# Kernel optimization log

Measured on AMD Instinct MI355X. Metric: run time of the kernel, lower is better.

The kernel has to match this reference:

```python
import jax, jax.numpy as jnp
import numpy as np

N = 100000
E = 600000
D = 128
D_OUT = 128
NUM_CONV = 3


def setup_inputs() -> dict:
    key = jax.random.key(0)
    k0, k1, k2, k3, k4, k5 = jax.random.split(key, 6)
    x = jax.random.normal(k0, (N, D), dtype=jnp.float32)
    edge_index = jax.random.randint(k1, (2, E), 0, N, dtype=jnp.int64)
    s = 1.0 / np.sqrt(D)
    W = jax.random.uniform(k2, (D, D), minval=-s, maxval=s, dtype=jnp.float32)
    b = jax.random.uniform(k3, (D,), minval=-s, maxval=s, dtype=jnp.float32)
    W_out = jax.random.uniform(k4, (D, D_OUT), minval=-s, maxval=s, dtype=jnp.float32)
    b_out = jax.random.uniform(k5, (D_OUT,), minval=-s, maxval=s, dtype=jnp.float32)
    return {"x": x, "edge_index": edge_index, "W": W, "b": b,
            "W_out": W_out, "b_out": b_out}


def reference(x, edge_index, W, b, W_out, b_out):
    src, dst = edge_index[0], edge_index[1]
    for _ in range(NUM_CONV):
        # gather messages from src nodes, scatter-sum into dst nodes
        agg = jax.ops.segment_sum(x[src], dst, num_segments=N)  # [N, D]
        x = jax.nn.relu(agg @ W + b)  # shared GCNLayer weights + ReLU
    return x @ W_out + b_out  # [N, D_OUT]
```

## Files before the change

### kernel.cpp

```cpp
#include <hip/hip_runtime.h>

#define NN 100000
#define NE 600000
#define DD 128


__global__ __launch_bounds__(256) void zero_kernel(int* __restrict__ p, int n) {
  int i = blockIdx.x * 256 + threadIdx.x;
  if (i < n) p[i] = 0;
}

__global__ __launch_bounds__(256) void count_deg(const int* __restrict__ dst, int* __restrict__ cnt) {
  int e = blockIdx.x * 256 + threadIdx.x;
  if (e < NE) atomicAdd(&cnt[dst[e]], 1);
}

__global__ __launch_bounds__(1024) void scan_partial(const int* __restrict__ cnt,
                                                     int* __restrict__ rowptr,
                                                     int* __restrict__ bsum) {
  __shared__ int tmp[2][1024];
  int t = threadIdx.x;
  int g = blockIdx.x * 1024 + t;
  int v = (g < NN) ? cnt[g] : 0;
  tmp[0][t] = v;
  __syncthreads();
  int pb = 0;
  for (int off = 1; off < 1024; off <<= 1) {
    int nv = tmp[pb][t] + ((t >= off) ? tmp[pb][t - off] : 0);
    tmp[1 - pb][t] = nv;
    pb ^= 1;
    __syncthreads();
  }
  int incl = tmp[pb][t];
  if (g < NN) rowptr[g] = incl - v;
  if (t == 1023) bsum[blockIdx.x] = incl;
}

__global__ void scan_sums(int* __restrict__ bsum, int nb) {
  if (threadIdx.x == 0 && blockIdx.x == 0) {
    int run = 0;
    for (int j = 0; j < nb; ++j) { int tv = bsum[j]; bsum[j] = run; run += tv; }
  }
}

__global__ __launch_bounds__(256) void scan_add(int* __restrict__ rowptr, const int* __restrict__ bsum) {
  int g = blockIdx.x * 256 + threadIdx.x;
  if (g < NN) rowptr[g] += bsum[g >> 10];
  if (g == 0) rowptr[NN] = NE;
}

__global__ __launch_bounds__(256) void fill_csr(const int* __restrict__ src, const int* __restrict__ dst,
                                                const int* __restrict__ rowptr, int* __restrict__ cur,
                                                int* __restrict__ srcidx) {
  int e = blockIdx.x * 256 + threadIdx.x;
  if (e < NE) {
    int d = dst[e];
    int pos = atomicAdd(&cur[d], 1);
    srcidx[rowptr[d] + pos] = src[e];
  }
}


__global__ __launch_bounds__(256) void aggregate(const float* __restrict__ y,
                                                 const int* __restrict__ rowptr,
                                                 const int* __restrict__ srcidx,
                                                 float* __restrict__ agg) {
  int grp  = (int)((blockIdx.x * 256 + threadIdx.x) >> 5);
  int lane = threadIdx.x & 31;
  if (grp >= NN) return;
  int beg = rowptr[grp], end = rowptr[grp + 1];
  float4 a0 = make_float4(0.f, 0.f, 0.f, 0.f);
  float4 a1 = make_float4(0.f, 0.f, 0.f, 0.f);
  int j = beg;
  for (; j + 2 <= end; j += 2) {
    int s0 = srcidx[j], s1 = srcidx[j + 1];
    float4 v0 = *(const float4*)(y + (size_t)s0 * DD + lane * 4);
    float4 v1 = *(const float4*)(y + (size_t)s1 * DD + lane * 4);
    a0.x += v0.x; a0.y += v0.y; a0.z += v0.z; a0.w += v0.w;
    a1.x += v1.x; a1.y += v1.y; a1.z += v1.z; a1.w += v1.w;
  }
  if (j < end) {
    int s0 = srcidx[j];
    float4 v0 = *(const float4*)(y + (size_t)s0 * DD + lane * 4);
    a0.x += v0.x; a0.y += v0.y; a0.z += v0.z; a0.w += v0.w;
  }
  float4 o = make_float4(a0.x + a1.x, a0.y + a1.y, a0.z + a1.z, a0.w + a1.w);
  *(float4*)(agg + (size_t)grp * DD + lane * 4) = o;
}


template <bool RELU>
__global__ __launch_bounds__(256) void gemm128(const float* __restrict__ A,
                                               const float* __restrict__ Wm,
                                               const float* __restrict__ bias,
                                               float* __restrict__ C, int nrows) {
  __shared__ float AsT[32][68];
  __shared__ float Ws[32][128];
  int t  = threadIdx.x;
  int tx = t & 15;
  int ty = t >> 4;
  int m0 = blockIdx.x * 64;
  float acc[4][8];
  #pragma unroll
  for (int r = 0; r < 4; ++r)
    #pragma unroll
    for (int c = 0; c < 8; ++c) acc[r][c] = 0.f;

  for (int kb = 0; kb < 4; ++kb) {
    #pragma unroll
    for (int i = 0; i < 2; ++i) {
      int q = t + i * 256;
      int m = q >> 3, k4 = q & 7;
      int row = m0 + m; if (row >= nrows) row = nrows - 1;
      float4 v = *(const float4*)(A + (size_t)row * DD + kb * 32 + k4 * 4);
      AsT[k4 * 4 + 0][m] = v.x;
      AsT[k4 * 4 + 1][m] = v.y;
      AsT[k4 * 4 + 2][m] = v.z;
      AsT[k4 * 4 + 3][m] = v.w;
    }
    #pragma unroll
    for (int i = 0; i < 4; ++i) {
      int q = t + i * 256;
      int kk = q >> 5, c4 = q & 31;
      *(float4*)(&Ws[kk][c4 * 4]) = *(const float4*)(Wm + (size_t)(kb * 32 + kk) * DD + c4 * 4);
    }
    __syncthreads();
    #pragma unroll
    for (int k = 0; k < 32; ++k) {
      float4 av = *(const float4*)(&AsT[k][ty * 4]);
      float4 w0 = *(const float4*)(&Ws[k][tx * 8]);
      float4 w1 = *(const float4*)(&Ws[k][tx * 8 + 4]);
      float a[4] = {av.x, av.y, av.z, av.w};
      float w[8] = {w0.x, w0.y, w0.z, w0.w, w1.x, w1.y, w1.z, w1.w};
      #pragma unroll
      for (int r = 0; r < 4; ++r)
        #pragma unroll
        for (int c = 0; c < 8; ++c) acc[r][c] += a[r] * w[c];
    }
    __syncthreads();
  }

  int c0 = tx * 8;
  float4 b0 = *(const float4*)(bias + c0);
  float4 b1 = *(const float4*)(bias + c0 + 4);
  float bb[8] = {b0.x, b0.y, b0.z, b0.w, b1.x, b1.y, b1.z, b1.w};
  #pragma unroll
  for (int r = 0; r < 4; ++r) {
    int row = m0 + ty * 4 + r;
    if (row < nrows) {
      float o[8];
      #pragma unroll
      for (int c = 0; c < 8; ++c) {
        float v = acc[r][c] + bb[c];
        o[c] = RELU ? fmaxf(v, 0.f) : v;
      }
      *(float4*)(C + (size_t)row * DD + c0)     = make_float4(o[0], o[1], o[2], o[3]);
      *(float4*)(C + (size_t)row * DD + c0 + 4) = make_float4(o[4], o[5], o[6], o[7]);
    }
  }
}


extern "C" void kernel_launch(void* const* d_in, const int* in_sizes, int n_in,
                              void* d_out, int out_size, void* d_ws, size_t ws_size,
                              hipStream_t stream) {
  const float* x     = (const float*)d_in[0];
  const int*   ei    = (const int*)d_in[1];
  const float* W     = (const float*)d_in[2];
  const float* b     = (const float*)d_in[3];
  const float* W_out = (const float*)d_in[4];
  const float* b_out = (const float*)d_in[5];
  float*       out   = (float*)d_out;

  const int* src = ei;
  const int* dst = ei + NE;

  char* ws = (char*)d_ws;
  int*   rowptr = (int*)(ws + 0);
  int*   cnt    = (int*)(ws + 400128);
  int*   bsum   = (int*)(ws + 800256);
  int*   srcidx = (int*)(ws + 802304);
  float* bufA   = (float*)(ws + 3202304);
  float* bufB   = (float*)(ws + 54402304);

  const int nb_scan = (NN + 1023) / 1024;

  zero_kernel<<<(NN + 255) / 256, 256, 0, stream>>>(cnt, NN);
  count_deg<<<(NE + 255) / 256, 256, 0, stream>>>(dst, cnt);
  scan_partial<<<nb_scan, 1024, 0, stream>>>(cnt, rowptr, bsum);
  scan_sums<<<1, 64, 0, stream>>>(bsum, nb_scan);
  scan_add<<<(NN + 255) / 256, 256, 0, stream>>>(rowptr, bsum);
  zero_kernel<<<(NN + 255) / 256, 256, 0, stream>>>(cnt, NN);
  fill_csr<<<(NE + 255) / 256, 256, 0, stream>>>(src, dst, rowptr, cnt, srcidx);

  const int aggBlocks  = (NN * 32 + 255) / 256;
  const int gemmBlocks = (NN + 63) / 64;

  aggregate<<<aggBlocks, 256, 0, stream>>>(x, rowptr, srcidx, bufA);
  gemm128<true><<<gemmBlocks, 256, 0, stream>>>(bufA, W, b, bufB, NN);
  aggregate<<<aggBlocks, 256, 0, stream>>>(bufB, rowptr, srcidx, bufA);
  gemm128<true><<<gemmBlocks, 256, 0, stream>>>(bufA, W, b, bufB, NN);
  aggregate<<<aggBlocks, 256, 0, stream>>>(bufB, rowptr, srcidx, bufA);
  gemm128<true><<<gemmBlocks, 256, 0, stream>>>(bufA, W, b, bufB, NN);
  gemm128<false><<<gemmBlocks, 256, 0, stream>>>(bufB, W_out, b_out, out, NN);
}
```

Measured before the change: 512.6 us.

## Replace FP32 SIMT GEMM with split-bf16 MFMA GEMM and bf16 hi/lo activations

Replaces the scalar FP32 GEMM with a matrix-core kernel that uses bf16x3 splitting (hi*hi + hi*lo + lo*hi) to keep near-FP32 accuracy. Aggregation now writes hi/lo bf16 halves directly, and the weights are pre-transposed and split once per call. The third layer writes its output in place as bf16 hi/lo, which feeds the output projection directly. Also moves the block-sum scan into shared memory. This triples the MFMA work and adds hi/lo traffic in exchange for much higher matrix-core throughput. The third layer's in-place overwrite of its input buffer relies on each block reading only its own rows.

```diff
diff --git a/kernel.cpp b/kernel.cpp
--- a/kernel.cpp
+++ b/kernel.cpp
@@ -3,6 +3,15 @@
 #define NN 100000
 #define NE 600000
 #define DD 128
+
+typedef __attribute__((ext_vector_type(8))) short bf16x8;
+typedef __attribute__((ext_vector_type(4))) float f32x4;
+
+__device__ __forceinline__ ushort f2bf(float f) {
+  uint u = __float_as_uint(f);
+  return (ushort)((u + 0x7FFF + ((u >> 16) & 1)) >> 16);
+}
+__device__ __forceinline__ float bf2f(ushort h) { return __uint_as_float(((uint)h) << 16); }
 
 
 __global__ __launch_bounds__(256) void zero_kernel(int* __restrict__ p, int n) {
@@ -36,11 +45,17 @@
   if (t == 1023) bsum[blockIdx.x] = incl;
 }
 
-__global__ void scan_sums(int* __restrict__ bsum, int nb) {
-  if (threadIdx.x == 0 && blockIdx.x == 0) {
+__global__ __launch_bounds__(128) void scan_sums(int* __restrict__ bsum, int nb) {
+  __shared__ int s[128];
+  int t = threadIdx.x;
+  s[t] = (t < nb) ? bsum[t] : 0;
+  __syncthreads();
+  if (t == 0) {
     int run = 0;
-    for (int j = 0; j < nb; ++j) { int tv = bsum[j]; bsum[j] = run; run += tv; }
-  }
+    for (int j = 0; j < nb; ++j) { int v = s[j]; s[j] = run; run += v; }
+  }
+  __syncthreads();
+  if (t < nb) bsum[t] = s[t];
 }
 
 __global__ __launch_bounds__(256) void scan_add(int* __restrict__ rowptr, const int* __restrict__ bsum) {
@@ -61,10 +76,25 @@
 }
 
 
+__global__ __launch_bounds__(256) void wprep(const float* __restrict__ W, const float* __restrict__ Wo,
+                                             ushort* __restrict__ WTh, ushort* __restrict__ WTl,
+                                             ushort* __restrict__ WToh, ushort* __restrict__ WTol) {
+  int i = blockIdx.x * 256 + threadIdx.x;
+  int j = i & 16383;
+  int k = j >> 7, n = j & 127;
+  float w = (i < 16384) ? W[j] : Wo[j];
+  ushort h = f2bf(w);
+  ushort lo = f2bf(w - bf2f(h));
+  int o = n * 128 + k;
+  if (i < 16384) { WTh[o] = h; WTl[o] = lo; }
+  else           { WToh[o] = h; WTol[o] = lo; }
+}
+
+
 __global__ __launch_bounds__(256) void aggregate(const float* __restrict__ y,
                                                  const int* __restrict__ rowptr,
                                                  const int* __restrict__ srcidx,
-                                                 float* __restrict__ agg) {
+                                                 ushort* __restrict__ Ah, ushort* __restrict__ Al) {
   int grp  = (int)((blockIdx.x * 256 + threadIdx.x) >> 5);
   int lane = threadIdx.x & 31;
   if (grp >= NN) return;
@@ -84,78 +114,100 @@
     float4 v0 = *(const float4*)(y + (size_t)s0 * DD + lane * 4);
     a0.x += v0.x; a0.y += v0.y; a0.z += v0.z; a0.w += v0.w;
   }
-  float4 o = make_float4(a0.x + a1.x, a0.y + a1.y, a0.z + a1.z, a0.w + a1.w);
-  *(float4*)(agg + (size_t)grp * DD + lane * 4) = o;
-}
-
-
-template <bool RELU>
-__global__ __launch_bounds__(256) void gemm128(const float* __restrict__ A,
-                                               const float* __restrict__ Wm,
-                                               const float* __restrict__ bias,
-                                               float* __restrict__ C, int nrows) {
-  __shared__ float AsT[32][68];
-  __shared__ float Ws[32][128];
-  int t  = threadIdx.x;
-  int tx = t & 15;
-  int ty = t >> 4;
-  int m0 = blockIdx.x * 64;
-  float acc[4][8];
-  #pragma unroll
-  for (int r = 0; r < 4; ++r)
-    #pragma unroll
-    for (int c = 0; c < 8; ++c) acc[r][c] = 0.f;
-
-  for (int kb = 0; kb < 4; ++kb) {
-    #pragma unroll
-    for (int i = 0; i < 2; ++i) {
-      int q = t + i * 256;
-      int m = q >> 3, k4 = q & 7;
-      int row = m0 + m; if (row >= nrows) row = nrows - 1;
-      float4 v = *(const float4*)(A + (size_t)row * DD + kb * 32 + k4 * 4);
-      AsT[k4 * 4 + 0][m] = v.x;
-      AsT[k4 * 4 + 1][m] = v.y;
-      AsT[k4 * 4 + 2][m] = v.z;
-      AsT[k4 * 4 + 3][m] = v.w;
-    }
+  float v[4] = {a0.x + a1.x, a0.y + a1.y, a0.z + a1.z, a0.w + a1.w};
+  ushort h[4], l[4];
+  #pragma unroll
+  for (int r = 0; r < 4; ++r) { h[r] = f2bf(v[r]); l[r] = f2bf(v[r] - bf2f(h[r])); }
+  uint2 hh, ll;
+  hh.x = (uint)h[0] | ((uint)h[1] << 16); hh.y = (uint)h[2] | ((uint)h[3] << 16);
+  ll.x = (uint)l[0] | ((uint)l[1] << 16); ll.y = (uint)l[2] | ((uint)l[3] << 16);
+  *(uint2*)(Ah + (size_t)grp * DD + lane * 4) = hh;
+  *(uint2*)(Al + (size_t)grp * DD + lane * 4) = ll;
+}
+
+
+template <int MODE>
+__global__ __launch_bounds__(256, 3) void gemm_mfma(const ushort* Ah, const ushort* Al,
+                                                    const ushort* __restrict__ Bh, const ushort* __restrict__ Bl,
+                                                    const float* __restrict__ bias,
+                                                    float* Cf, ushort* Ch, ushort* Cl, int nrows) {
+  __shared__ ushort BHs[128 * 64];
+  __shared__ ushort BLs[128 * 64];
+  int t = threadIdx.x;
+  int w = t >> 6, l = t & 63;
+  int lrow = l & 15, g = l >> 4;
+  int m0 = blockIdx.x * 128 + w * 32;
+
+  f32x4 acc[2][8];
+  #pragma unroll
+  for (int rt = 0; rt < 2; ++rt)
+    #pragma unroll
+    for (int ct = 0; ct < 8; ++ct) acc[rt][ct] = (f32x4){0.f, 0.f, 0.f, 0.f};
+
+  #pragma unroll
+  for (int p = 0; p < 2; ++p) {
     #pragma unroll
     for (int i = 0; i < 4; ++i) {
-      int q = t + i * 256;
-      int kk = q >> 5, c4 = q & 31;
-      *(float4*)(&Ws[kk][c4 * 4]) = *(const float4*)(Wm + (size_t)(kb * 32 + kk) * DD + c4 * 4);
+      int c = t + i * 256;
+      int n = c >> 3, k8 = c & 7;
+      int gsrc = n * 128 + p * 64 + k8 * 8;
+      int dsw  = n * 64 + (((k8 * 16) ^ ((n & 7) << 4)) >> 1);
+      *(uint4*)(&BHs[dsw]) = *(const uint4*)(Bh + gsrc);
+      *(uint4*)(&BLs[dsw]) = *(const uint4*)(Bl + gsrc);
     }
     __syncthreads();
-    #pragma unroll
-    for (int k = 0; k < 32; ++k) {
-      float4 av = *(const float4*)(&AsT[k][ty * 4]);
-      float4 w0 = *(const float4*)(&Ws[k][tx * 8]);
-      float4 w1 = *(const float4*)(&Ws[k][tx * 8 + 4]);
-      float a[4] = {av.x, av.y, av.z, av.w};
-      float w[8] = {w0.x, w0.y, w0.z, w0.w, w1.x, w1.y, w1.z, w1.w};
+
+    #pragma unroll
+    for (int kb = 0; kb < 2; ++kb) {
+      int kgl = (p * 2 + kb) * 32 + g * 8;
+      bf16x8 ah[2], al[2];
       #pragma unroll
-      for (int r = 0; r < 4; ++r)
+      for (int rt = 0; rt < 2; ++rt) {
+        int row = m0 + rt * 16 + lrow; if (row >= nrows) row = nrows - 1;
+        ah[rt] = *(const bf16x8*)(Ah + (size_t)row * DD + kgl);
+        al[rt] = *(const bf16x8*)(Al + (size_t)row * DD + kgl);
+      }
+      int kloc = kb * 64 + g * 16;
+      int swz = (lrow & 7) << 4;
+      #pragma unroll
+      for (int ct = 0; ct < 8; ++ct) {
+        int off = (ct * 16 + lrow) * 64 + ((kloc ^ swz) >> 1);
+        bf16x8 bh = *(const bf16x8*)(&BHs[off]);
+        bf16x8 bl = *(const bf16x8*)(&BLs[off]);
         #pragma unroll
-        for (int c = 0; c < 8; ++c) acc[r][c] += a[r] * w[c];
+        for (int rt = 0; rt < 2; ++rt) {
+          acc[rt][ct] = __builtin_amdgcn_mfma_f32_16x16x32_bf16(ah[rt], bh, acc[rt][ct], 0, 0, 0);
+          acc[rt][ct] = __builtin_amdgcn_mfma_f32_16x16x32_bf16(ah[rt], bl, acc[rt][ct], 0, 0, 0);
+          acc[rt][ct] = __builtin_amdgcn_mfma_f32_16x16x32_bf16(al[rt], bh, acc[rt][ct], 0, 0, 0);
+        }
+      }
     }
     __syncthreads();
   }
 
-  int c0 = tx * 8;
-  float4 b0 = *(const float4*)(bias + c0);
-  float4 b1 = *(const float4*)(bias + c0 + 4);
-  float bb[8] = {b0.x, b0.y, b0.z, b0.w, b1.x, b1.y, b1.z, b1.w};
-  #pragma unroll
-  for (int r = 0; r < 4; ++r) {
-    int row = m0 + ty * 4 + r;
-    if (row < nrows) {
-      float o[8];
-      #pragma unroll
-      for (int c = 0; c < 8; ++c) {
-        float v = acc[r][c] + bb[c];
-        o[c] = RELU ? fmaxf(v, 0.f) : v;
+  float bb[8];
+  #pragma unroll
+  for (int ct = 0; ct < 8; ++ct) bb[ct] = bias[ct * 16 + lrow];
+  #pragma unroll
+  for (int rt = 0; rt < 2; ++rt) {
+    #pragma unroll
+    for (int r = 0; r < 4; ++r) {
+      int row = m0 + rt * 16 + g * 4 + r;
+      if (row < nrows) {
+        #pragma unroll
+        for (int ct = 0; ct < 8; ++ct) {
+          float v = acc[rt][ct][r] + bb[ct];
+          if (MODE != 2) v = fmaxf(v, 0.f);
+          int col = ct * 16 + lrow;
+          if (MODE == 1) {
+            ushort h = f2bf(v);
+            Ch[(size_t)row * DD + col] = h;
+            Cl[(size_t)row * DD + col] = f2bf(v - bf2f(h));
+          } else {
+            Cf[(size_t)row * DD + col] = v;
+          }
+        }
       }
-      *(float4*)(C + (size_t)row * DD + c0)     = make_float4(o[0], o[1], o[2], o[3]);
-      *(float4*)(C + (size_t)row * DD + c0 + 4) = make_float4(o[4], o[5], o[6], o[7]);
     }
   }
 }
@@ -176,31 +228,37 @@
   const int* dst = ei + NE;
 
   char* ws = (char*)d_ws;
-  int*   rowptr = (int*)(ws + 0);
-  int*   cnt    = (int*)(ws + 400128);
-  int*   bsum   = (int*)(ws + 800256);
-  int*   srcidx = (int*)(ws + 802304);
-  float* bufA   = (float*)(ws + 3202304);
-  float* bufB   = (float*)(ws + 54402304);
+  int*    rowptr = (int*)(ws + 0);
+  int*    cnt    = (int*)(ws + 400128);
+  int*    bsum   = (int*)(ws + 800256);
+  int*    srcidx = (int*)(ws + 802304);
+  ushort* WTh    = (ushort*)(ws + 3202304);
+  ushort* WTl    = (ushort*)(ws + 3235072);
+  ushort* WToh   = (ushort*)(ws + 3267840);
+  ushort* WTol   = (ushort*)(ws + 3300608);
+  ushort* Ahb    = (ushort*)(ws + 3333376);
+  ushort* Alb    = (ushort*)(ws + 28933376);
+  float*  yf     = (float*)(ws + 54533376);
 
   const int nb_scan = (NN + 1023) / 1024;
 
   zero_kernel<<<(NN + 255) / 256, 256, 0, stream>>>(cnt, NN);
   count_deg<<<(NE + 255) / 256, 256, 0, stream>>>(dst, cnt);
   scan_partial<<<nb_scan, 1024, 0, stream>>>(cnt, rowptr, bsum);
-  scan_sums<<<1, 64, 0, stream>>>(bsum, nb_scan);
+  scan_sums<<<1, 128, 0, stream>>>(bsum, nb_scan);
   scan_add<<<(NN + 255) / 256, 256, 0, stream>>>(rowptr, bsum);
   zero_kernel<<<(NN + 255) / 256, 256, 0, stream>>>(cnt, NN);
   fill_csr<<<(NE + 255) / 256, 256, 0, stream>>>(src, dst, rowptr, cnt, srcidx);
+  wprep<<<128, 256, 0, stream>>>(W, W_out, WTh, WTl, WToh, WTol);
 
   const int aggBlocks  = (NN * 32 + 255) / 256;
-  const int gemmBlocks = (NN + 63) / 64;
-
-  aggregate<<<aggBlocks, 256, 0, stream>>>(x, rowptr, srcidx, bufA);
-  gemm128<true><<<gemmBlocks, 256, 0, stream>>>(bufA, W, b, bufB, NN);
-  aggregate<<<aggBlocks, 256, 0, stream>>>(bufB, rowptr, srcidx, bufA);
-  gemm128<true><<<gemmBlocks, 256, 0, stream>>>(bufA, W, b, bufB, NN);
-  aggregate<<<aggBlocks, 256, 0, stream>>>(bufB, rowptr, srcidx, bufA);
-  gemm128<true><<<gemmBlocks, 256, 0, stream>>>(bufA, W, b, bufB, NN);
-  gemm128<false><<<gemmBlocks, 256, 0, stream>>>(bufB, W_out, b_out, out, NN);
-}
+  const int gemmBlocks = (NN + 127) / 128;
+
+  aggregate<<<aggBlocks, 256, 0, stream>>>(x, rowptr, srcidx, Ahb, Alb);
+  gemm_mfma<0><<<gemmBlocks, 256, 0, stream>>>(Ahb, Alb, WTh, WTl, b, yf, nullptr, nullptr, NN);
+  aggregate<<<aggBlocks, 256, 0, stream>>>(yf, rowptr, srcidx, Ahb, Alb);
+  gemm_mfma<0><<<gemmBlocks, 256, 0, stream>>>(Ahb, Alb, WTh, WTl, b, yf, nullptr, nullptr, NN);
+  aggregate<<<aggBlocks, 256, 0, stream>>>(yf, rowptr, srcidx, Ahb, Alb);
+  gemm_mfma<1><<<gemmBlocks, 256, 0, stream>>>(Ahb, Alb, WTh, WTl, b, nullptr, Ahb, Alb, NN);
+  gemm_mfma<2><<<gemmBlocks, 256, 0, stream>>>(Ahb, Alb, WToh, WTol, b_out, out, nullptr, nullptr, NN);
+}
```

Measured after the change: 413.6 us. 19.3% less time.
